# Performance work log

Hardware: AMD Instinct MI355X
Metric: run time of the kernel (lower is better)

## Reference

```python
import jax, jax.numpy as jnp
import numpy as np

N = 100000   # nodes
E = 3200000  # edges
F = 128      # num_features
H = 20       # hidden dim (hard-coded in source)
C = 10       # num_classes
EPS = 1e-5


def setup_inputs() -> dict:
    key = jax.random.key(0)
    ks = jax.random.split(key, 16)
    x = jax.random.normal(ks[0], (N, F), jnp.float32)
    edge_index = jax.random.randint(ks[1], (2, E), 0, N)
    edge_weights = jnp.ones((E,), jnp.float32)

    def lin_init(k, fan_in, shape):
        s = 1.0 / np.sqrt(fan_in)
        return jax.random.uniform(k, shape, jnp.float32, -s, s)

    return {
        "x": x,
        "edge_index": edge_index,
        "edge_weights": edge_weights,
        "W1": lin_init(ks[2], F, (F, H)), "b1": jnp.zeros((H,), jnp.float32),
        "g1": jnp.ones((H,), jnp.float32), "be1": jnp.zeros((H,), jnp.float32),
        "W2": lin_init(ks[3], H, (H, H)), "b2": jnp.zeros((H,), jnp.float32),
        "g2": jnp.ones((H,), jnp.float32), "be2": jnp.zeros((H,), jnp.float32),
        "W3": lin_init(ks[4], H, (H, H)), "b3": jnp.zeros((H,), jnp.float32),
        "Wl": lin_init(ks[5], 3 * H, (3 * H, C)), "bl": lin_init(ks[6], 3 * H, (C,)),
    }


def gcn_conv(x, src, dst, ew, W, b, n):
    # PyG GCNConv: transform, add self-loops, symmetric deg^-1/2 normalization, scatter-add.
    h = x @ W  # [N, out]
    loop = jnp.arange(n)
    src2 = jnp.concatenate([src, loop])
    dst2 = jnp.concatenate([dst, loop])
    ew2 = jnp.concatenate([ew, jnp.ones((n,), x.dtype)])
    deg = jax.ops.segment_sum(ew2, dst2, num_segments=n)
    dinv = jnp.where(deg > 0, jax.lax.rsqrt(deg), 0.0)
    coef = (dinv[src2] * ew2 * dinv[dst2])[:, None]  # [E+N, 1]
    out = jax.ops.segment_sum(h[src2] * coef, dst2, num_segments=n)
    return out + b


def batch_norm(x, g, b):
    m = x.mean(axis=0)
    v = x.var(axis=0)
    return (x - m) * jax.lax.rsqrt(v + EPS) * g + b


def reference(x, edge_index, edge_weights, W1, b1, g1, be1, W2, b2, g2, be2, W3, b3, Wl, bl):
    src, dst = edge_index[0], edge_index[1]
    n = x.shape[0]
    o1 = batch_norm(jax.nn.relu(gcn_conv(x, src, dst, edge_weights, W1, b1, n)), g1, be1)
    o2 = batch_norm(jax.nn.relu(gcn_conv(o1, src, dst, edge_weights, W2, b2, n)), g2, be2)
    o3 = jax.nn.relu(gcn_conv(o2, src, dst, edge_weights, W3, b3, n))
    emb = jnp.concatenate([o1, o2, o3], axis=1)  # [N, 60]
    return emb @ Wl + bl
```

## Files before the change

### kernel.cpp

```cpp
#include <hip/hip_runtime.h>
#include <hip/hip_bf16.h>
#include <hip/hip_fp16.h>


#define HD 20
#define EPS 1e-5f
#define BSH 7
#define NBMAX 1024
#define CAP 5632

__global__ __launch_bounds__(1024)
void init_kernel(int* bcnt, float* stats, float* zero20, int nbv) {
    int t = threadIdx.x;
    if (t < nbv) bcnt[t] = 0;
    if (t < 80) stats[t] = 0.0f;
    if (t < HD) zero20[t] = 0.0f;
}

__global__ __launch_bounds__(256)
void bucket_hist_kernel(const int* __restrict__ dst, int* __restrict__ bcnt,
                        int E, int chunk, int nbv) {
    __shared__ int lh[NBMAX];
    for (int i = threadIdx.x; i < nbv; i += 256) lh[i] = 0;
    __syncthreads();
    int s = blockIdx.x * chunk;
    int e = s + chunk; if (e > E) e = E;
    for (int j = s + threadIdx.x; j < e; j += 256)
        atomicAdd(&lh[dst[j] >> BSH], 1);
    __syncthreads();
    for (int i = threadIdx.x; i < nbv; i += 256)
        if (lh[i]) atomicAdd(&bcnt[i], lh[i]);
}

__global__ __launch_bounds__(1024)
void bucket_scan_kernel(const int* __restrict__ bcnt, int* __restrict__ bstart,
                        int* __restrict__ bcur, int* __restrict__ row_start,
                        int n, int E, int nbv) {
    __shared__ int s[1024];
    int t = threadIdx.x;
    int v = (t < nbv) ? bcnt[t] : 0;
    s[t] = v;
    __syncthreads();
    for (int off = 1; off < 1024; off <<= 1) {
        int u = (t >= off) ? s[t - off] : 0;
        __syncthreads();
        s[t] += u;
        __syncthreads();
    }
    if (t < nbv) { int st = s[t] - v; bstart[t] = st; bcur[t] = st; }
    if (t == 0) { bstart[nbv] = E; row_start[n] = E; }
}

__global__ __launch_bounds__(256)
void scatter_kernel(const int* __restrict__ src, const int* __restrict__ dst,
                    const float* __restrict__ ew, int* __restrict__ bcur,
                    int2* __restrict__ tmp, int E, int chunk, int nbv) {
    __shared__ int lh[NBMAX];
    __shared__ int lbase[NBMAX];
    for (int i = threadIdx.x; i < nbv; i += 256) lh[i] = 0;
    __syncthreads();
    int s = blockIdx.x * chunk;
    int e = s + chunk; if (e > E) e = E;
    for (int j = s + threadIdx.x; j < e; j += 256)
        atomicAdd(&lh[dst[j] >> BSH], 1);
    __syncthreads();
    for (int i = threadIdx.x; i < nbv; i += 256) {
        int c = lh[i];
        lbase[i] = c ? atomicAdd(&bcur[i], c) : 0;
        lh[i] = 0;
    }
    __syncthreads();
    for (int j = s + threadIdx.x; j < e; j += 256) {
        int d = dst[j];
        int b = d >> BSH;
        int pos = atomicAdd(&lh[b], 1);
        tmp[lbase[b] + pos] = make_int2(src[j] | ((d & ((1 << BSH) - 1)) << 20),
                                        __float_as_int(ew[j]));
    }
}

__global__ __launch_bounds__(256)
void finalize_kernel(const int2* __restrict__ tmp, const int* __restrict__ bstart,
                     int2* __restrict__ se, int* __restrict__ row_start,
                     float* __restrict__ dinv, int n) {
    __shared__ int hist[128];
    __shared__ float degs[128];
    __shared__ int off[128];
    __shared__ int cur[128];
    __shared__ int2 stage[CAP];
    int b = blockIdx.x;
    int s0 = bstart[b], s1 = bstart[b + 1];
    int cnt = s1 - s0;
    int t = threadIdx.x;
    if (t < 128) { hist[t] = 0; degs[t] = 0.0f; cur[t] = 0; }
    __syncthreads();
    for (int j = s0 + t; j < s1; j += 256) {
        int2 r = tmp[j];
        int l = r.x >> 20;
        atomicAdd(&hist[l], 1);
        atomicAdd(&degs[l], __int_as_float(r.y));
    }
    __syncthreads();
    if (t < 128) off[t] = hist[t];
    __syncthreads();
    for (int o = 1; o < 128; o <<= 1) {
        int u = (t < 128 && t >= o) ? off[t - o] : 0;
        __syncthreads();
        if (t < 128) off[t] += u;
        __syncthreads();
    }
    if (t < 128) {
        int node = (b << BSH) + t;
        if (node < n) {
            row_start[node] = s0 + off[t] - hist[t];
            dinv[node] = rsqrtf(1.0f + degs[t]);
        }
    }
    __syncthreads();
    if (cnt <= CAP) {
        for (int j = s0 + t; j < s1; j += 256) {
            int2 r = tmp[j];
            int l = r.x >> 20;
            int p = (off[l] - hist[l]) + atomicAdd(&cur[l], 1);
            stage[p] = make_int2(r.x & 0xFFFFF, r.y);
        }
        __syncthreads();
        for (int k = t; k < cnt; k += 256) se[s0 + k] = stage[k];
    } else {
        for (int j = s0 + t; j < s1; j += 256) {
            int2 r = tmp[j];
            int l = r.x >> 20;
            int p = (off[l] - hist[l]) + atomicAdd(&cur[l], 1);
            se[s0 + p] = make_int2(r.x & 0xFFFFF, r.y);
        }
    }
}

template<int FIN, int NPB>
__global__ __launch_bounds__(256)
void gemm_kernel(const float* __restrict__ in, const float* __restrict__ W,
                 const float* __restrict__ cvec, const float* __restrict__ dinv,
                 __half* __restrict__ hs, int n) {
    __shared__ float sWt[HD][FIN + 4];
    __shared__ float sIn[NPB][FIN + 4];
    __shared__ float sC[HD];
    for (int i = threadIdx.x; i < FIN * HD; i += 256) {
        int k = i / HD, f = i % HD;
        sWt[f][k] = W[i];
    }
    if (threadIdx.x < HD) sC[threadIdx.x] = cvec[threadIdx.x];
    int base = blockIdx.x * NPB;
    int nb = n - base; if (nb > NPB) nb = NPB;
    int lim = n * FIN;
    const int Q = FIN / 4;
    for (int i = threadIdx.x; i < NPB * Q; i += 256) {
        int row = i / Q, c = (i % Q) * 4;
        int g = (base + row) * FIN + c;
        *(float4*)&sIn[row][c] = (g < lim) ? *(const float4*)&in[g]
                                           : make_float4(0.f, 0.f, 0.f, 0.f);
    }
    __syncthreads();
    for (int idx = threadIdx.x; idx < NPB * HD; idx += 256) {
        int nl = idx / HD, f = idx % HD;
        float4 a = make_float4(0.f, 0.f, 0.f, 0.f);
        #pragma unroll 4
        for (int k = 0; k < FIN; k += 4) {
            float4 x4 = *(const float4*)&sIn[nl][k];
            float4 w4 = *(const float4*)&sWt[f][k];
            a.x = fmaf(x4.x, w4.x, a.x);
            a.y = fmaf(x4.y, w4.y, a.y);
            a.z = fmaf(x4.z, w4.z, a.z);
            a.w = fmaf(x4.w, w4.w, a.w);
        }
        if (nl < nb)
            hs[(base + nl) * HD + f] = __float2half_rn(
                (((a.x + a.y) + (a.z + a.w)) + sC[f]) * dinv[base + nl]);
    }
}

#define FMA4(A, V, W) \
    A.x = fmaf(V.x, W, A.x); A.y = fmaf(V.y, W, A.y); \
    A.z = fmaf(V.z, W, A.z); A.w = fmaf(V.w, W, A.w);

__device__ __forceinline__ float4 h4f2(uint2 u) {
    float2 f0 = __half22float2(*reinterpret_cast<const __half2*>(&u.x));
    float2 f1 = __half22float2(*reinterpret_cast<const __half2*>(&u.y));
    return make_float4(f0.x, f0.y, f1.x, f1.y);
}

template<int MODE>
__global__ __launch_bounds__(256)
void agg_kernel(const uint2* __restrict__ hs4, const float* __restrict__ dinv,
                const int* __restrict__ row_start, const int2* __restrict__ se,
                const float* __restrict__ bias, float* __restrict__ out,
                float* __restrict__ stat_sum, float* __restrict__ stat_sq,
                const float* __restrict__ o1, const float* __restrict__ o2,
                const float* __restrict__ Wlp, const float* __restrict__ blp,
                int n) {
    __shared__ float ls[HD], lq[HD];
    __shared__ float sW[600];
    __shared__ float sb[10];
    if (MODE == 0) {
        if (threadIdx.x < HD) { ls[threadIdx.x] = 0.0f; lq[threadIdx.x] = 0.0f; }
        __syncthreads();
    } else {
        for (int i = threadIdx.x; i < 600; i += 256) sW[i] = Wlp[i];
        if (threadIdx.x < 10) sb[threadIdx.x] = blp[threadIdx.x];
        __syncthreads();
    }
    int t = blockIdx.x * blockDim.x + threadIdx.x;
    int i = t >> 2, lane = t & 3;
    if (i < n) {
        float di = dinv[i];
        int s0 = row_start[i], s1 = row_start[i + 1];
        float4 a0, a1, a2, a3, a4;
        if (lane == 0) {
            const uint2* s = hs4 + i * 5;
            a0 = h4f2(s[0]); a1 = h4f2(s[1]); a2 = h4f2(s[2]);
            a3 = h4f2(s[3]); a4 = h4f2(s[4]);
        } else {
            a0 = a1 = a2 = a3 = a4 = make_float4(0.f, 0.f, 0.f, 0.f);
        }
        int j = s0 + lane;
        if (j < s1) {
            int2 e = se[j];
            float w = __int_as_float(e.y);
            const uint2* r = hs4 + e.x * 5;
            uint2 c0 = r[0], c1 = r[1], c2 = r[2], c3 = r[3], c4 = r[4];
            while (true) {
                int jn = j + 4;
                bool more = jn < s1;
                int jp = more ? jn : j;
                int2 en = se[jp];
                const uint2* rn = hs4 + en.x * 5;
                uint2 n0 = rn[0], n1 = rn[1], n2 = rn[2], n3 = rn[3], n4 = rn[4];
                float wn = __int_as_float(en.y);
                float4 v0 = h4f2(c0), v1 = h4f2(c1), v2 = h4f2(c2);
                float4 v3 = h4f2(c3), v4 = h4f2(c4);
                FMA4(a0, v0, w) FMA4(a1, v1, w) FMA4(a2, v2, w)
                FMA4(a3, v3, w) FMA4(a4, v4, w)
                if (!more) break;
                j = jn; w = wn;
                c0 = n0; c1 = n1; c2 = n2; c3 = n3; c4 = n4;
            }
        }
        #define REDX(A, M) \
            A.x += __shfl_xor(A.x, M); A.y += __shfl_xor(A.y, M); \
            A.z += __shfl_xor(A.z, M); A.w += __shfl_xor(A.w, M);
        #define RED4L(A) REDX(A, 1) REDX(A, 2)
        RED4L(a0) RED4L(a1) RED4L(a2) RED4L(a3) RED4L(a4)
        float4 acc[5] = {a0, a1, a2, a3, a4};
        float va[HD];
        #pragma unroll
        for (int q = 0; q < 5; ++q) {
            float4 bb = *(const float4*)(bias + 4 * q);
            va[4 * q + 0] = fmaxf(fmaf(acc[q].x, di, bb.x), 0.0f);
            va[4 * q + 1] = fmaxf(fmaf(acc[q].y, di, bb.y), 0.0f);
            va[4 * q + 2] = fmaxf(fmaf(acc[q].z, di, bb.z), 0.0f);
            va[4 * q + 3] = fmaxf(fmaf(acc[q].w, di, bb.w), 0.0f);
        }
        if (MODE == 0) {
            if (lane == 0) {
                #pragma unroll
                for (int q = 0; q < 5; ++q) {
                    ((float4*)out)[i * 5 + q] = make_float4(
                        va[4 * q], va[4 * q + 1], va[4 * q + 2], va[4 * q + 3]);
                    int f = 4 * q;
                    atomicAdd(&ls[f + 0], va[f + 0]); atomicAdd(&lq[f + 0], va[f + 0] * va[f + 0]);
                    atomicAdd(&ls[f + 1], va[f + 1]); atomicAdd(&lq[f + 1], va[f + 1] * va[f + 1]);
                    atomicAdd(&ls[f + 2], va[f + 2]); atomicAdd(&lq[f + 2], va[f + 2] * va[f + 2]);
                    atomicAdd(&ls[f + 3], va[f + 3]); atomicAdd(&lq[f + 3], va[f + 3] * va[f + 3]);
                }
            }
        } else {
            float r1[HD], r2[HD];
            #pragma unroll
            for (int q = 0; q < 5; ++q) {
                *(float4*)&r1[4 * q] = ((const float4*)(o1 + (size_t)i * HD))[q];
                *(float4*)&r2[4 * q] = ((const float4*)(o2 + (size_t)i * HD))[q];
            }
            for (int c = lane; c < 10; c += 4) {
                float s = sb[c];
                #pragma unroll
                for (int k = 0; k < HD; ++k) s = fmaf(r1[k], sW[k * 10 + c], s);
                #pragma unroll
                for (int k = 0; k < HD; ++k) s = fmaf(r2[k], sW[(HD + k) * 10 + c], s);
                #pragma unroll
                for (int k = 0; k < HD; ++k) s = fmaf(va[k], sW[(2 * HD + k) * 10 + c], s);
                out[(size_t)i * 10 + c] = s;
            }
        }
    }
    if (MODE == 0) {
        __syncthreads();
        if (threadIdx.x < HD) {
            atomicAdd(&stat_sum[threadIdx.x], ls[threadIdx.x]);
            atomicAdd(&stat_sq[threadIdx.x], lq[threadIdx.x]);
        }
    }
}

__global__ __launch_bounds__(512)
void bn_adjust_kernel(const float* __restrict__ sum, const float* __restrict__ sq,
                      const float* __restrict__ g, const float* __restrict__ be,
                      const float* __restrict__ W, float* __restrict__ scsh_out,
                      float* __restrict__ Wp, float* __restrict__ cvec, int n) {
    __shared__ float ssc[HD], ssh[HD];
    int t = threadIdx.x;
    if (t < HD) {
        float inv_n = 1.0f / (float)n;
        float m = sum[t] * inv_n;
        float var = sq[t] * inv_n - m * m;
        float sc = g[t] * rsqrtf(var + EPS);
        float sh = be[t] - m * sc;
        ssc[t] = sc; ssh[t] = sh;
        scsh_out[t] = sc; scsh_out[HD + t] = sh;
    }
    __syncthreads();
    if (t < HD * HD) Wp[t] = ssc[t / HD] * W[t];
    if (t < HD) {
        float acc = 0.0f;
        #pragma unroll
        for (int k = 0; k < HD; ++k) acc = fmaf(ssh[k], W[k * HD + t], acc);
        cvec[t] = acc;
    }
}

__global__ __launch_bounds__(640)
void bn_adjust2_kernel(const float* __restrict__ sum, const float* __restrict__ sq,
                       const float* __restrict__ g, const float* __restrict__ be,
                       const float* __restrict__ W, float* __restrict__ scsh_out,
                       float* __restrict__ Wp, float* __restrict__ cvec,
                       const float* __restrict__ Wl, const float* __restrict__ bl,
                       const float* __restrict__ scsh1,
                       float* __restrict__ Wlp, float* __restrict__ blp, int n) {
    __shared__ float ssc[HD], ssh[HD];
    int t = threadIdx.x;
    if (t < HD) {
        float inv_n = 1.0f / (float)n;
        float m = sum[t] * inv_n;
        float var = sq[t] * inv_n - m * m;
        float sc = g[t] * rsqrtf(var + EPS);
        float sh = be[t] - m * sc;
        ssc[t] = sc; ssh[t] = sh;
        scsh_out[t] = sc; scsh_out[HD + t] = sh;
    }
    __syncthreads();
    if (t < HD * HD) Wp[t] = ssc[t / HD] * W[t];
    if (t < HD) {
        float acc = 0.0f;
        #pragma unroll
        for (int k = 0; k < HD; ++k) acc = fmaf(ssh[k], W[k * HD + t], acc);
        cvec[t] = acc;
    }
    if (t < 600) {
        int k = t / 10;
        float s = (k < HD) ? scsh1[k] : (k < 2 * HD) ? ssc[k - HD] : 1.0f;
        Wlp[t] = s * Wl[t];
    }
    if (t < 10) {
        float acc = bl[t];
        #pragma unroll
        for (int k = 0; k < HD; ++k) acc = fmaf(scsh1[HD + k], Wl[k * 10 + t], acc);
        #pragma unroll
        for (int k = 0; k < HD; ++k) acc = fmaf(ssh[k], Wl[(HD + k) * 10 + t], acc);
        blp[t] = acc;
    }
}

extern "C" void kernel_launch(void* const* d_in, const int* in_sizes, int n_in,
                              void* d_out, int out_size, void* d_ws, size_t ws_size,
                              hipStream_t stream) {
    const float* x   = (const float*)d_in[0];
    const int*   ei  = (const int*)d_in[1];
    const float* ew  = (const float*)d_in[2];
    const float* W1  = (const float*)d_in[3];
    const float* b1  = (const float*)d_in[4];
    const float* g1  = (const float*)d_in[5];
    const float* be1 = (const float*)d_in[6];
    const float* W2  = (const float*)d_in[7];
    const float* b2  = (const float*)d_in[8];
    const float* g2  = (const float*)d_in[9];
    const float* be2 = (const float*)d_in[10];
    const float* W3  = (const float*)d_in[11];
    const float* b3  = (const float*)d_in[12];
    const float* Wl  = (const float*)d_in[13];
    const float* bl  = (const float*)d_in[14];
    float* out = (float*)d_out;

    const int F = in_sizes[3] / HD;
    const int N = in_sizes[0] / F;
    const int E = in_sizes[2];
    const int* src = ei;
    const int* dst = ei + E;
    const int nbv = (N + 127) >> BSH;

    char* p = (char*)d_ws;
    auto alloc = [&](size_t bytes) -> void* {
        void* r = (void*)p;
        p += (bytes + 255) & ~(size_t)255;
        return r;
    };
    size_t nh4 = (size_t)N * HD * 4;
    int2*  se      = (int2*) alloc((size_t)E * 8);
    char*  regionA = (char*) alloc((size_t)E * 8);
    float* o2r     = (float*)alloc(nh4);
    float* dinv    = (float*)alloc((size_t)N * 4);
    int*   row_start = (int*)alloc((size_t)(N + 1) * 4);
    int*   bcnt    = (int*)  alloc(NBMAX * 4);
    int*   bstart  = (int*)  alloc((NBMAX + 1) * 4);
    int*   bcur    = (int*)  alloc(NBMAX * 4);
    float* stats   = (float*)alloc(80 * 4);
    float* scsh    = (float*)alloc(80 * 4);
    float* zero20  = (float*)alloc(20 * 4);
    float* W2p     = (float*)alloc(400 * 4);
    float* c2      = (float*)alloc(20 * 4);
    float* W3p     = (float*)alloc(400 * 4);
    float* c3      = (float*)alloc(20 * 4);
    float* Wlp     = (float*)alloc(600 * 4);
    float* blp     = (float*)alloc(12 * 4);

    int2*   tmp = (int2*)regionA;
    __half* hs  = (__half*)regionA;
    float*  o1r = (float*)(regionA + 2 * nh4);

    const int B = 256;
    const int GB = 512;
    const int chunk = (E + GB - 1) / GB;
    int gAgg = (4 * N + B - 1) / B;

    hipLaunchKernelGGL(init_kernel, dim3(1), dim3(1024), 0, stream, bcnt, stats, zero20, nbv);
    hipLaunchKernelGGL(bucket_hist_kernel, dim3(GB), dim3(B), 0, stream, dst, bcnt, E, chunk, nbv);
    hipLaunchKernelGGL(bucket_scan_kernel, dim3(1), dim3(1024), 0, stream,
                       bcnt, bstart, bcur, row_start, N, E, nbv);
    hipLaunchKernelGGL(scatter_kernel, dim3(GB), dim3(B), 0, stream,
                       src, dst, ew, bcur, tmp, E, chunk, nbv);
    hipLaunchKernelGGL(finalize_kernel, dim3(nbv), dim3(B), 0, stream,
                       tmp, bstart, se, row_start, dinv, N);

    hipLaunchKernelGGL((gemm_kernel<128, 16>), dim3((N + 15) / 16), dim3(B), 0, stream,
                       x, W1, zero20, dinv, hs, N);
    hipLaunchKernelGGL((agg_kernel<0>), dim3(gAgg), dim3(B), 0, stream,
                       (const uint2*)hs, dinv, row_start, se, b1, o1r,
                       stats, stats + 20, nullptr, nullptr, nullptr, nullptr, N);
    hipLaunchKernelGGL(bn_adjust_kernel, dim3(1), dim3(512), 0, stream,
                       stats, stats + 20, g1, be1, W2, scsh, W2p, c2, N);

    hipLaunchKernelGGL((gemm_kernel<HD, 64>), dim3((N + 63) / 64), dim3(B), 0, stream,
                       o1r, W2p, c2, dinv, hs, N);
    hipLaunchKernelGGL((agg_kernel<0>), dim3(gAgg), dim3(B), 0, stream,
                       (const uint2*)hs, dinv, row_start, se, b2, o2r,
                       stats + 40, stats + 60, nullptr, nullptr, nullptr, nullptr, N);
    hipLaunchKernelGGL(bn_adjust2_kernel, dim3(1), dim3(640), 0, stream,
                       stats + 40, stats + 60, g2, be2, W3, scsh + 40, W3p, c3,
                       Wl, bl, scsh, Wlp, blp, N);

    hipLaunchKernelGGL((gemm_kernel<HD, 64>), dim3((N + 63) / 64), dim3(B), 0, stream,
                       o2r, W3p, c3, dinv, hs, N);
    hipLaunchKernelGGL((agg_kernel<1>), dim3(gAgg), dim3(B), 0, stream,
                       (const uint2*)hs, dinv, row_start, se, b3, out,
                       nullptr, nullptr, o1r, o2r, Wlp, blp, N);
}
```

Measured before the change: 551.1 us.

## Aggregate per 128-node bucket with LDS atomics instead of full CSR sort

Drops the per-node CSR finalize step (local counting sort and row_start) and keeps only bucket-sorted edges plus a lighter degree kernel. Each aggregation block now handles one 128-node bucket, streaming its edges and accumulating into a shared-memory [128][21] tile with float atomics, then applies bias, ReLU, BN statistics or the final linear layer. The hidden features are padded to 24 halves so each row loads as aligned uint4 chunks. The aim is to remove the finalize pass and its extra edge-array traffic, at the cost of many shared-memory atomics per edge and a nondeterministic summation order.

Measured after the change: 1.572 ms. 185% more time.

```diff
diff --git a/kernel.cpp b/kernel.cpp
--- a/kernel.cpp
+++ b/kernel.cpp
@@ -1,13 +1,13 @@
 #include <hip/hip_runtime.h>
-#include <hip/hip_bf16.h>
 #include <hip/hip_fp16.h>
 
 
 #define HD 20
+#define HSS 24
 #define EPS 1e-5f
 #define BSH 7
 #define NBMAX 1024
-#define CAP 5632
+#define AGT 512
 
 __global__ __launch_bounds__(1024)
 void init_kernel(int* bcnt, float* stats, float* zero20, int nbv) {
@@ -34,8 +34,7 @@
 
 __global__ __launch_bounds__(1024)
 void bucket_scan_kernel(const int* __restrict__ bcnt, int* __restrict__ bstart,
-                        int* __restrict__ bcur, int* __restrict__ row_start,
-                        int n, int E, int nbv) {
+                        int* __restrict__ bcur, int E, int nbv) {
     __shared__ int s[1024];
     int t = threadIdx.x;
     int v = (t < nbv) ? bcnt[t] : 0;
@@ -48,7 +47,7 @@
         __syncthreads();
     }
     if (t < nbv) { int st = s[t] - v; bstart[t] = st; bcur[t] = st; }
-    if (t == 0) { bstart[nbv] = E; row_start[n] = E; }
+    if (t == 0) bstart[nbv] = E;
 }
 
 __global__ __launch_bounds__(256)
@@ -80,59 +79,22 @@
 }
 
 __global__ __launch_bounds__(256)
-void finalize_kernel(const int2* __restrict__ tmp, const int* __restrict__ bstart,
-                     int2* __restrict__ se, int* __restrict__ row_start,
-                     float* __restrict__ dinv, int n) {
-    __shared__ int hist[128];
+void deg_kernel(const int2* __restrict__ tmp, const int* __restrict__ bstart,
+                float* __restrict__ dinv, int n) {
     __shared__ float degs[128];
-    __shared__ int off[128];
-    __shared__ int cur[128];
-    __shared__ int2 stage[CAP];
     int b = blockIdx.x;
+    int t = threadIdx.x;
+    if (t < 128) degs[t] = 0.0f;
+    __syncthreads();
     int s0 = bstart[b], s1 = bstart[b + 1];
-    int cnt = s1 - s0;
-    int t = threadIdx.x;
-    if (t < 128) { hist[t] = 0; degs[t] = 0.0f; cur[t] = 0; }
-    __syncthreads();
     for (int j = s0 + t; j < s1; j += 256) {
         int2 r = tmp[j];
-        int l = r.x >> 20;
-        atomicAdd(&hist[l], 1);
-        atomicAdd(&degs[l], __int_as_float(r.y));
-    }
-    __syncthreads();
-    if (t < 128) off[t] = hist[t];
-    __syncthreads();
-    for (int o = 1; o < 128; o <<= 1) {
-        int u = (t < 128 && t >= o) ? off[t - o] : 0;
-        __syncthreads();
-        if (t < 128) off[t] += u;
-        __syncthreads();
-    }
+        atomicAdd(&degs[r.x >> 20], __int_as_float(r.y));
+    }
+    __syncthreads();
     if (t < 128) {
         int node = (b << BSH) + t;
-        if (node < n) {
-            row_start[node] = s0 + off[t] - hist[t];
-            dinv[node] = rsqrtf(1.0f + degs[t]);
-        }
-    }
-    __syncthreads();
-    if (cnt <= CAP) {
-        for (int j = s0 + t; j < s1; j += 256) {
-            int2 r = tmp[j];
-            int l = r.x >> 20;
-            int p = (off[l] - hist[l]) + atomicAdd(&cur[l], 1);
-            stage[p] = make_int2(r.x & 0xFFFFF, r.y);
-        }
-        __syncthreads();
-        for (int k = t; k < cnt; k += 256) se[s0 + k] = stage[k];
-    } else {
-        for (int j = s0 + t; j < s1; j += 256) {
-            int2 r = tmp[j];
-            int l = r.x >> 20;
-            int p = (off[l] - hist[l]) + atomicAdd(&cur[l], 1);
-            se[s0 + p] = make_int2(r.x & 0xFFFFF, r.y);
-        }
+        if (node < n) dinv[node] = rsqrtf(1.0f + degs[t]);
     }
 }
 
@@ -173,129 +135,142 @@
             a.w = fmaf(x4.w, w4.w, a.w);
         }
         if (nl < nb)
-            hs[(base + nl) * HD + f] = __float2half_rn(
+            hs[(size_t)(base + nl) * HSS + f] = __float2half_rn(
                 (((a.x + a.y) + (a.z + a.w)) + sC[f]) * dinv[base + nl]);
     }
 }
 
-#define FMA4(A, V, W) \
-    A.x = fmaf(V.x, W, A.x); A.y = fmaf(V.y, W, A.y); \
-    A.z = fmaf(V.z, W, A.z); A.w = fmaf(V.w, W, A.w);
-
-__device__ __forceinline__ float4 h4f2(uint2 u) {
-    float2 f0 = __half22float2(*reinterpret_cast<const __half2*>(&u.x));
-    float2 f1 = __half22float2(*reinterpret_cast<const __half2*>(&u.y));
-    return make_float4(f0.x, f0.y, f1.x, f1.y);
+__device__ __forceinline__ float2 h2f(unsigned u) {
+    return __half22float2(*reinterpret_cast<const __half2*>(&u));
 }
 
 template<int MODE>
-__global__ __launch_bounds__(256)
-void agg_kernel(const uint2* __restrict__ hs4, const float* __restrict__ dinv,
-                const int* __restrict__ row_start, const int2* __restrict__ se,
+__global__ __launch_bounds__(AGT)
+void agg_kernel(const uint4* __restrict__ hs4, const float* __restrict__ dinv,
+                const int2* __restrict__ tmp, const int* __restrict__ bstart,
                 const float* __restrict__ bias, float* __restrict__ out,
                 float* __restrict__ stat_sum, float* __restrict__ stat_sq,
                 const float* __restrict__ o1, const float* __restrict__ o2,
                 const float* __restrict__ Wlp, const float* __restrict__ blp,
                 int n) {
-    __shared__ float ls[HD], lq[HD];
+    __shared__ float acc[128][21];
+    __shared__ float sbias[HD];
     __shared__ float sW[600];
     __shared__ float sb[10];
+    int t = threadIdx.x, b = blockIdx.x;
+    for (int i = t; i < 128 * 21; i += AGT) ((float*)acc)[i] = 0.0f;
+    if (t < HD) sbias[t] = bias[t];
+    if (MODE == 1) {
+        for (int i = t; i < 600; i += AGT) sW[i] = Wlp[i];
+        if (t < 10) sb[t] = blp[t];
+    }
+    __syncthreads();
+
+    int s0 = bstart[b], s1 = bstart[b + 1];
+    int j = s0 + t;
+    if (j < s1) {
+        int2 e = tmp[j];
+        const uint4* r = hs4 + (size_t)(e.x & 0xFFFFF) * 3;
+        uint4 c0 = r[0], c1 = r[1];
+        uint2 c2 = *(const uint2*)(r + 2);
+        while (true) {
+            int jn = j + AGT;
+            bool more = jn < s1;
+            int jp = more ? jn : j;
+            int2 en = tmp[jp];
+            const uint4* rn = hs4 + (size_t)(en.x & 0xFFFFF) * 3;
+            uint4 n0 = rn[0], n1 = rn[1];
+            uint2 n2 = *(const uint2*)(rn + 2);
+            float w = __int_as_float(e.y);
+            float* a = acc[e.x >> 20];
+            #define ACC2(U, F) { float2 v_ = h2f(U); \
+                atomicAdd(a + (F), w * v_.x); atomicAdd(a + (F) + 1, w * v_.y); }
+            ACC2(c0.x, 0)  ACC2(c0.y, 2)  ACC2(c0.z, 4)  ACC2(c0.w, 6)
+            ACC2(c1.x, 8)  ACC2(c1.y, 10) ACC2(c1.z, 12) ACC2(c1.w, 14)
+            ACC2(c2.x, 16) ACC2(c2.y, 18)
+            #undef ACC2
+            if (!more) break;
+            j = jn; e = en;
+            c0 = n0; c1 = n1; c2 = n2;
+        }
+    }
+    __syncthreads();
+
     if (MODE == 0) {
-        if (threadIdx.x < HD) { ls[threadIdx.x] = 0.0f; lq[threadIdx.x] = 0.0f; }
-        __syncthreads();
-    } else {
-        for (int i = threadIdx.x; i < 600; i += 256) sW[i] = Wlp[i];
-        if (threadIdx.x < 10) sb[threadIdx.x] = blp[threadIdx.x];
-        __syncthreads();
-    }
-    int t = blockIdx.x * blockDim.x + threadIdx.x;
-    int i = t >> 2, lane = t & 3;
-    if (i < n) {
-        float di = dinv[i];
-        int s0 = row_start[i], s1 = row_start[i + 1];
-        float4 a0, a1, a2, a3, a4;
-        if (lane == 0) {
-            const uint2* s = hs4 + i * 5;
-            a0 = h4f2(s[0]); a1 = h4f2(s[1]); a2 = h4f2(s[2]);
-            a3 = h4f2(s[3]); a4 = h4f2(s[4]);
-        } else {
-            a0 = a1 = a2 = a3 = a4 = make_float4(0.f, 0.f, 0.f, 0.f);
-        }
-        int j = s0 + lane;
-        if (j < s1) {
-            int2 e = se[j];
-            float w = __int_as_float(e.y);
-            const uint2* r = hs4 + e.x * 5;
-            uint2 c0 = r[0], c1 = r[1], c2 = r[2], c3 = r[3], c4 = r[4];
-            while (true) {
-                int jn = j + 4;
-                bool more = jn < s1;
-                int jp = more ? jn : j;
-                int2 en = se[jp];
-                const uint2* rn = hs4 + en.x * 5;
-                uint2 n0 = rn[0], n1 = rn[1], n2 = rn[2], n3 = rn[3], n4 = rn[4];
-                float wn = __int_as_float(en.y);
-                float4 v0 = h4f2(c0), v1 = h4f2(c1), v2 = h4f2(c2);
-                float4 v3 = h4f2(c3), v4 = h4f2(c4);
-                FMA4(a0, v0, w) FMA4(a1, v1, w) FMA4(a2, v2, w)
-                FMA4(a3, v3, w) FMA4(a4, v4, w)
-                if (!more) break;
-                j = jn; w = wn;
-                c0 = n0; c1 = n1; c2 = n2; c3 = n3; c4 = n4;
+        if (t < 128) {
+            int i = (b << BSH) + t;
+            if (i < n) {
+                float di = dinv[i];
+                const uint4* r = hs4 + (size_t)i * 3;
+                uint4 q0 = r[0], q1 = r[1];
+                uint2 q2 = *(const uint2*)(r + 2);
+                float sf[HD];
+                #define UNP(U, F) { float2 v_ = h2f(U); sf[F] = v_.x; sf[(F)+1] = v_.y; }
+                UNP(q0.x, 0)  UNP(q0.y, 2)  UNP(q0.z, 4)  UNP(q0.w, 6)
+                UNP(q1.x, 8)  UNP(q1.y, 10) UNP(q1.z, 12) UNP(q1.w, 14)
+                UNP(q2.x, 16) UNP(q2.y, 18)
+                float va[HD];
+                #pragma unroll
+                for (int f = 0; f < HD; ++f)
+                    va[f] = fmaxf((acc[t][f] + sf[f]) * di + sbias[f], 0.0f);
+                float4* op = (float4*)(out + (size_t)i * HD);
+                #pragma unroll
+                for (int q = 0; q < 5; ++q)
+                    op[q] = make_float4(va[4*q], va[4*q+1], va[4*q+2], va[4*q+3]);
+                #pragma unroll
+                for (int f = 0; f < HD; ++f) acc[t][f] = va[f];
+                #undef UNP
             }
         }
-        #define REDX(A, M) \
-            A.x += __shfl_xor(A.x, M); A.y += __shfl_xor(A.y, M); \
-            A.z += __shfl_xor(A.z, M); A.w += __shfl_xor(A.w, M);
-        #define RED4L(A) REDX(A, 1) REDX(A, 2)
-        RED4L(a0) RED4L(a1) RED4L(a2) RED4L(a3) RED4L(a4)
-        float4 acc[5] = {a0, a1, a2, a3, a4};
-        float va[HD];
-        #pragma unroll
-        for (int q = 0; q < 5; ++q) {
-            float4 bb = *(const float4*)(bias + 4 * q);
-            va[4 * q + 0] = fmaxf(fmaf(acc[q].x, di, bb.x), 0.0f);
-            va[4 * q + 1] = fmaxf(fmaf(acc[q].y, di, bb.y), 0.0f);
-            va[4 * q + 2] = fmaxf(fmaf(acc[q].z, di, bb.z), 0.0f);
-            va[4 * q + 3] = fmaxf(fmaf(acc[q].w, di, bb.w), 0.0f);
+        __syncthreads();
+        if (t < HD) {
+            float s = 0.0f, q = 0.0f;
+            #pragma unroll 8
+            for (int nl = 0; nl < 128; ++nl) {
+                float v = acc[nl][t];
+                s += v; q += v * v;
+            }
+            atomicAdd(&stat_sum[t], s);
+            atomicAdd(&stat_sq[t], q);
         }
-        if (MODE == 0) {
-            if (lane == 0) {
+    } else {
+        if (t < 128) {
+            int i = (b << BSH) + t;
+            if (i < n) {
+                float di = dinv[i];
+                const uint4* r = hs4 + (size_t)i * 3;
+                uint4 q0 = r[0], q1 = r[1];
+                uint2 q2 = *(const uint2*)(r + 2);
+                float sf[HD];
+                #define UNP(U, F) { float2 v_ = h2f(U); sf[F] = v_.x; sf[(F)+1] = v_.y; }
+                UNP(q0.x, 0)  UNP(q0.y, 2)  UNP(q0.z, 4)  UNP(q0.w, 6)
+                UNP(q1.x, 8)  UNP(q1.y, 10) UNP(q1.z, 12) UNP(q1.w, 14)
+                UNP(q2.x, 16) UNP(q2.y, 18)
+                #undef UNP
+                float va[HD];
+                #pragma unroll
+                for (int f = 0; f < HD; ++f)
+                    va[f] = fmaxf((acc[t][f] + sf[f]) * di + sbias[f], 0.0f);
+                float r1[HD], r2[HD];
+                const float4* p1 = (const float4*)(o1 + (size_t)i * HD);
+                const float4* p2 = (const float4*)(o2 + (size_t)i * HD);
                 #pragma unroll
                 for (int q = 0; q < 5; ++q) {
-                    ((float4*)out)[i * 5 + q] = make_float4(
-                        va[4 * q], va[4 * q + 1], va[4 * q + 2], va[4 * q + 3]);
-                    int f = 4 * q;
-                    atomicAdd(&ls[f + 0], va[f + 0]); atomicAdd(&lq[f + 0], va[f + 0] * va[f + 0]);
-                    atomicAdd(&ls[f + 1], va[f + 1]); atomicAdd(&lq[f + 1], va[f + 1] * va[f + 1]);
-                    atomicAdd(&ls[f + 2], va[f + 2]); atomicAdd(&lq[f + 2], va[f + 2] * va[f + 2]);
-                    atomicAdd(&ls[f + 3], va[f + 3]); atomicAdd(&lq[f + 3], va[f + 3] * va[f + 3]);
+                    *(float4*)&r1[4*q] = p1[q];
+                    *(float4*)&r2[4*q] = p2[q];
+                }
+                #pragma unroll
+                for (int c = 0; c < 10; ++c) {
+                    float s = sb[c];
+                    #pragma unroll
+                    for (int k = 0; k < HD; ++k) s = fmaf(r1[k], sW[k * 10 + c], s);
+                    #pragma unroll
+                    for (int k = 0; k < HD; ++k) s = fmaf(r2[k], sW[(HD + k) * 10 + c], s);
+                    #pragma unroll
+                    for (int k = 0; k < HD; ++k) s = fmaf(va[k], sW[(2 * HD + k) * 10 + c], s);
+                    out[(size_t)i * 10 + c] = s;
                 }
             }
-        } else {
-            float r1[HD], r2[HD];
-            #pragma unroll
-            for (int q = 0; q < 5; ++q) {
-                *(float4*)&r1[4 * q] = ((const float4*)(o1 + (size_t)i * HD))[q];
-                *(float4*)&r2[4 * q] = ((const float4*)(o2 + (size_t)i * HD))[q];
-            }
-            for (int c = lane; c < 10; c += 4) {
-                float s = sb[c];
-                #pragma unroll
-                for (int k = 0; k < HD; ++k) s = fmaf(r1[k], sW[k * 10 + c], s);
-                #pragma unroll
-                for (int k = 0; k < HD; ++k) s = fmaf(r2[k], sW[(HD + k) * 10 + c], s);
-                #pragma unroll
-                for (int k = 0; k < HD; ++k) s = fmaf(va[k], sW[(2 * HD + k) * 10 + c], s);
-                out[(size_t)i * 10 + c] = s;
-            }
-        }
-    }
-    if (MODE == 0) {
-        __syncthreads();
-        if (threadIdx.x < HD) {
-            atomicAdd(&stat_sum[threadIdx.x], ls[threadIdx.x]);
-            atomicAdd(&stat_sq[threadIdx.x], lq[threadIdx.x]);
         }
     }
 }
@@ -401,12 +376,11 @@
         p += (bytes + 255) & ~(size_t)255;
         return r;
     };
-    size_t nh4 = (size_t)N * HD * 4;
-    int2*  se      = (int2*) alloc((size_t)E * 8);
-    char*  regionA = (char*) alloc((size_t)E * 8);
-    float* o2r     = (float*)alloc(nh4);
-    float* dinv    = (float*)alloc((size_t)N * 4);
-    int*   row_start = (int*)alloc((size_t)(N + 1) * 4);
+    int2*   tmp  = (int2*)  alloc((size_t)E * 8);
+    __half* hs   = (__half*)alloc((size_t)N * HSS * 2);
+    float*  o1r  = (float*) alloc((size_t)N * HD * 4);
+    float*  o2r  = (float*) alloc((size_t)N * HD * 4);
+    float*  dinv = (float*) alloc((size_t)N * 4);
     int*   bcnt    = (int*)  alloc(NBMAX * 4);
     int*   bstart  = (int*)  alloc((NBMAX + 1) * 4);
     int*   bcur    = (int*)  alloc(NBMAX * 4);
@@ -420,36 +394,32 @@
     float* Wlp     = (float*)alloc(600 * 4);
     float* blp     = (float*)alloc(12 * 4);
 
-    int2*   tmp = (int2*)regionA;
-    __half* hs  = (__half*)regionA;
-    float*  o1r = (float*)(regionA + 2 * nh4);
+    const uint4* hs4 = (const uint4*)hs;
 
     const int B = 256;
     const int GB = 512;
     const int chunk = (E + GB - 1) / GB;
-    int gAgg = (4 * N + B - 1) / B;
 
     hipLaunchKernelGGL(init_kernel, dim3(1), dim3(1024), 0, stream, bcnt, stats, zero20, nbv);
     hipLaunchKernelGGL(bucket_hist_kernel, dim3(GB), dim3(B), 0, stream, dst, bcnt, E, chunk, nbv);
     hipLaunchKernelGGL(bucket_scan_kernel, dim3(1), dim3(1024), 0, stream,
-                       bcnt, bstart, bcur, row_start, N, E, nbv);
+                       bcnt, bstart, bcur, E, nbv);
     hipLaunchKernelGGL(scatter_kernel, dim3(GB), dim3(B), 0, stream,
                        src, dst, ew, bcur, tmp, E, chunk, nbv);
-    hipLaunchKernelGGL(finalize_kernel, dim3(nbv), dim3(B), 0, stream,
-                       tmp, bstart, se, row_start, dinv, N);
+    hipLaunchKernelGGL(deg_kernel, dim3(nbv), dim3(B), 0, stream, tmp, bstart, dinv, N);
 
     hipLaunchKernelGGL((gemm_kernel<128, 16>), dim3((N + 15) / 16), dim3(B), 0, stream,
                        x, W1, zero20, dinv, hs, N);
-    hipLaunchKernelGGL((agg_kernel<0>), dim3(gAgg), dim3(B), 0, stream,
-                       (const uint2*)hs, dinv, row_start, se, b1, o1r,
+    hipLaunchKernelGGL((agg_kernel<0>), dim3(nbv), dim3(AGT), 0, stream,
+                       hs4, dinv, tmp, bstart, b1, o1r,
                        stats, stats + 20, nullptr, nullptr, nullptr, nullptr, N);
     hipLaunchKernelGGL(bn_adjust_kernel, dim3(1), dim3(512), 0, stream,
                        stats, stats + 20, g1, be1, W2, scsh, W2p, c2, N);
 
     hipLaunchKernelGGL((gemm_kernel<HD, 64>), dim3((N + 63) / 64), dim3(B), 0, stream,
                        o1r, W2p, c2, dinv, hs, N);
-    hipLaunchKernelGGL((agg_kernel<0>), dim3(gAgg), dim3(B), 0, stream,
-                       (const uint2*)hs, dinv, row_start, se, b2, o2r,
+    hipLaunchKernelGGL((agg_kernel<0>), dim3(nbv), dim3(AGT), 0, stream,
+                       hs4, dinv, tmp, bstart, b2, o2r,
                        stats + 40, stats + 60, nullptr, nullptr, nullptr, nullptr, N);
     hipLaunchKernelGGL(bn_adjust2_kernel, dim3(1), dim3(640), 0, stream,
                        stats + 40, stats + 60, g2, be2, W3, scsh + 40, W3p, c3,
@@ -457,7 +427,7 @@
 
     hipLaunchKernelGGL((gemm_kernel<HD, 64>), dim3((N + 63) / 64), dim3(B), 0, stream,
                        o2r, W3p, c3, dinv, hs, N);
-    hipLaunchKernelGGL((agg_kernel<1>), dim3(gAgg), dim3(B), 0, stream,
-                       (const uint2*)hs, dinv, row_start, se, b3, out,
+    hipLaunchKernelGGL((agg_kernel<1>), dim3(nbv), dim3(AGT), 0, stream,
+                       hs4, dinv, tmp, bstart, b3, out,
                        nullptr, nullptr, o1r, o2r, Wlp, blp, N);
 }
```

## Pad fp16 hidden rows to 24 halves and use 8 lanes per node in aggregation

Applied to the files above, without the earlier changes.

Hidden feature rows in fp16 are stored with a stride of 24 halves, so each gathered row is fetched with two 16-byte loads plus one 8-byte load instead of five 8-byte loads. The aggregation kernel now assigns 8 lanes per destination node instead of 4, with a three-step shuffle reduction. This aims to cut the per-edge gather instruction count and expose more memory-level parallelism on the gather-bound aggregation. In exchange it needs a larger intermediate buffer that may run into the following region, wastes some lanes on low-degree nodes, and launches twice as many threads.

After: 594.2 us. 7.8% more time.

```diff
diff --git a/kernel.cpp b/kernel.cpp
--- a/kernel.cpp
+++ b/kernel.cpp
@@ -1,13 +1,14 @@
 #include <hip/hip_runtime.h>
-#include <hip/hip_bf16.h>
 #include <hip/hip_fp16.h>
 
 
 #define HD 20
+#define HSS 24
 #define EPS 1e-5f
 #define BSH 7
 #define NBMAX 1024
 #define CAP 5632
+#define LPN 8
 
 __global__ __launch_bounds__(1024)
 void init_kernel(int* bcnt, float* stats, float* zero20, int nbv) {
@@ -173,7 +174,7 @@
             a.w = fmaf(x4.w, w4.w, a.w);
         }
         if (nl < nb)
-            hs[(base + nl) * HD + f] = __float2half_rn(
+            hs[(size_t)(base + nl) * HSS + f] = __float2half_rn(
                 (((a.x + a.y) + (a.z + a.w)) + sC[f]) * dinv[base + nl]);
     }
 }
@@ -190,7 +191,7 @@
 
 template<int MODE>
 __global__ __launch_bounds__(256)
-void agg_kernel(const uint2* __restrict__ hs4, const float* __restrict__ dinv,
+void agg_kernel(const uint4* __restrict__ hs4, const float* __restrict__ dinv,
                 const int* __restrict__ row_start, const int2* __restrict__ se,
                 const float* __restrict__ bias, float* __restrict__ out,
                 float* __restrict__ stat_sum, float* __restrict__ stat_sq,
@@ -209,15 +210,20 @@
         __syncthreads();
     }
     int t = blockIdx.x * blockDim.x + threadIdx.x;
-    int i = t >> 2, lane = t & 3;
+    int i = t >> 3, lane = t & (LPN - 1);
     if (i < n) {
         float di = dinv[i];
         int s0 = row_start[i], s1 = row_start[i + 1];
         float4 a0, a1, a2, a3, a4;
         if (lane == 0) {
-            const uint2* s = hs4 + i * 5;
-            a0 = h4f2(s[0]); a1 = h4f2(s[1]); a2 = h4f2(s[2]);
-            a3 = h4f2(s[3]); a4 = h4f2(s[4]);
+            const uint4* s = hs4 + (size_t)i * 3;
+            uint4 q0 = s[0], q1 = s[1];
+            uint2 q2 = *(const uint2*)(s + 2);
+            a0 = h4f2(make_uint2(q0.x, q0.y));
+            a1 = h4f2(make_uint2(q0.z, q0.w));
+            a2 = h4f2(make_uint2(q1.x, q1.y));
+            a3 = h4f2(make_uint2(q1.z, q1.w));
+            a4 = h4f2(q2);
         } else {
             a0 = a1 = a2 = a3 = a4 = make_float4(0.f, 0.f, 0.f, 0.f);
         }
@@ -225,30 +231,35 @@
         if (j < s1) {
             int2 e = se[j];
             float w = __int_as_float(e.y);
-            const uint2* r = hs4 + e.x * 5;
-            uint2 c0 = r[0], c1 = r[1], c2 = r[2], c3 = r[3], c4 = r[4];
+            const uint4* r = hs4 + (size_t)e.x * 3;
+            uint4 c0 = r[0], c1 = r[1];
+            uint2 c2 = *(const uint2*)(r + 2);
             while (true) {
-                int jn = j + 4;
+                int jn = j + LPN;
                 bool more = jn < s1;
                 int jp = more ? jn : j;
                 int2 en = se[jp];
-                const uint2* rn = hs4 + en.x * 5;
-                uint2 n0 = rn[0], n1 = rn[1], n2 = rn[2], n3 = rn[3], n4 = rn[4];
+                const uint4* rn = hs4 + (size_t)en.x * 3;
+                uint4 n0 = rn[0], n1 = rn[1];
+                uint2 n2 = *(const uint2*)(rn + 2);
                 float wn = __int_as_float(en.y);
-                float4 v0 = h4f2(c0), v1 = h4f2(c1), v2 = h4f2(c2);
-                float4 v3 = h4f2(c3), v4 = h4f2(c4);
+                float4 v0 = h4f2(make_uint2(c0.x, c0.y));
+                float4 v1 = h4f2(make_uint2(c0.z, c0.w));
+                float4 v2 = h4f2(make_uint2(c1.x, c1.y));
+                float4 v3 = h4f2(make_uint2(c1.z, c1.w));
+                float4 v4 = h4f2(c2);
                 FMA4(a0, v0, w) FMA4(a1, v1, w) FMA4(a2, v2, w)
                 FMA4(a3, v3, w) FMA4(a4, v4, w)
                 if (!more) break;
                 j = jn; w = wn;
-                c0 = n0; c1 = n1; c2 = n2; c3 = n3; c4 = n4;
+                c0 = n0; c1 = n1; c2 = n2;
             }
         }
         #define REDX(A, M) \
             A.x += __shfl_xor(A.x, M); A.y += __shfl_xor(A.y, M); \
             A.z += __shfl_xor(A.z, M); A.w += __shfl_xor(A.w, M);
-        #define RED4L(A) REDX(A, 1) REDX(A, 2)
-        RED4L(a0) RED4L(a1) RED4L(a2) RED4L(a3) RED4L(a4)
+        #define RED8L(A) REDX(A, 1) REDX(A, 2) REDX(A, 4)
+        RED8L(a0) RED8L(a1) RED8L(a2) RED8L(a3) RED8L(a4)
         float4 acc[5] = {a0, a1, a2, a3, a4};
         float va[HD];
         #pragma unroll
@@ -279,7 +290,7 @@
                 *(float4*)&r1[4 * q] = ((const float4*)(o1 + (size_t)i * HD))[q];
                 *(float4*)&r2[4 * q] = ((const float4*)(o2 + (size_t)i * HD))[q];
             }
-            for (int c = lane; c < 10; c += 4) {
+            for (int c = lane; c < 10; c += LPN) {
                 float s = sb[c];
                 #pragma unroll
                 for (int k = 0; k < HD; ++k) s = fmaf(r1[k], sW[k * 10 + c], s);
@@ -424,10 +435,12 @@
     __half* hs  = (__half*)regionA;
     float*  o1r = (float*)(regionA + 2 * nh4);
 
+    const uint4* hs4 = (const uint4*)hs;
+
     const int B = 256;
     const int GB = 512;
     const int chunk = (E + GB - 1) / GB;
-    int gAgg = (4 * N + B - 1) / B;
+    int gAgg = (LPN * N + B - 1) / B;
 
     hipLaunchKernelGGL(init_kernel, dim3(1), dim3(1024), 0, stream, bcnt, stats, zero20, nbv);
     hipLaunchKernelGGL(bucket_hist_kernel, dim3(GB), dim3(B), 0, stream, dst, bcnt, E, chunk, nbv);
@@ -441,7 +454,7 @@
     hipLaunchKernelGGL((gemm_kernel<128, 16>), dim3((N + 15) / 16), dim3(B), 0, stream,
                        x, W1, zero20, dinv, hs, N);
     hipLaunchKernelGGL((agg_kernel<0>), dim3(gAgg), dim3(B), 0, stream,
-                       (const uint2*)hs, dinv, row_start, se, b1, o1r,
+                       hs4, dinv, row_start, se, b1, o1r,
                        stats, stats + 20, nullptr, nullptr, nullptr, nullptr, N);
     hipLaunchKernelGGL(bn_adjust_kernel, dim3(1), dim3(512), 0, stream,
                        stats, stats + 20, g1, be1, W2, scsh, W2p, c2, N);
@@ -449,7 +462,7 @@
     hipLaunchKernelGGL((gemm_kernel<HD, 64>), dim3((N + 63) / 64), dim3(B), 0, stream,
                        o1r, W2p, c2, dinv, hs, N);
     hipLaunchKernelGGL((agg_kernel<0>), dim3(gAgg), dim3(B), 0, stream,
-                       (const uint2*)hs, dinv, row_start, se, b2, o2r,
+                       hs4, dinv, row_start, se, b2, o2r,
                        stats + 40, stats + 60, nullptr, nullptr, nullptr, nullptr, N);
     hipLaunchKernelGGL(bn_adjust2_kernel, dim3(1), dim3(640), 0, stream,
                        stats + 40, stats + 60, g2, be2, W3, scsh + 40, W3p, c3,
@@ -458,6 +471,6 @@
     hipLaunchKernelGGL((gemm_kernel<HD, 64>), dim3((N + 63) / 64), dim3(B), 0, stream,
                        o2r, W3p, c3, dinv, hs, N);
     hipLaunchKernelGGL((agg_kernel<1>), dim3(gAgg), dim3(B), 0, stream,
-                       (const uint2*)hs, dinv, row_start, se, b3, out,
+                       hs4, dinv, row_start, se, b3, out,
                        nullptr, nullptr, o1r, o2r, Wlp, blp, N);
 }
```
